# Kernel optimization log

Measured on AMD Instinct MI355X. Metric: run time of the kernel, lower is better.

## Reference

```python
import jax, jax.numpy as jnp
import numpy as np

EPS = 1e-05
H, N, F = 1024, 16, 4096  # hidden_dim, state_dim, ffn_dim


def layernorm(x, g, b):
    mu = jnp.mean(x, axis=-1, keepdims=True)
    var = jnp.mean(jnp.square(x - mu), axis=-1, keepdims=True)
    return (x - mu) * jax.lax.rsqrt(var + EPS) * g + b


def setup_inputs() -> dict:
    key = jax.random.key(0)
    ks = jax.random.split(key, 12)
    B, L = 2, 2048
    s = lambda fan_in: 1.0 / np.sqrt(fan_in)
    inp = {
        "x": jax.random.normal(ks[0], (B, L, H), jnp.float32),
        "ln1_g": jnp.ones((H,), jnp.float32),
        "ln1_b": jnp.zeros((H,), jnp.float32),
        "Wd": jax.random.uniform(ks[1], (H, H), jnp.float32, -s(H), s(H)),
        "bd": jnp.zeros((H,), jnp.float32),
        "Wbc": jax.random.uniform(ks[2], (2 * N, H), jnp.float32, -s(H), s(H)),
        "bbc": jnp.zeros((2 * N,), jnp.float32),
        "A_log": jnp.log(jnp.tile(jnp.arange(1, N + 1, dtype=jnp.float32), (H, 1))),
        "D": jnp.ones((H,), jnp.float32),
        "ln2_g": jnp.ones((H,), jnp.float32),
        "ln2_b": jnp.zeros((H,), jnp.float32),
        "W1": jax.random.uniform(ks[3], (F, H), jnp.float32, -s(H), s(H)),
        "b1": jnp.zeros((F,), jnp.float32),
        "W2": jax.random.uniform(ks[4], (H, F), jnp.float32, -s(F), s(F)),
        "b2": jnp.zeros((H,), jnp.float32),
    }
    return inp


def _selective_ssm(xn, delta, Bm, Cm, A, D):
    # xn: (B,L,H)  delta: (B,L,H)  Bm,Cm: (B,L,N)  A: (H,N)  D: (H,)
    Bsz = xn.shape[0]
    # time-major for scan
    xs = (jnp.moveaxis(delta, 1, 0), jnp.moveaxis(Bm, 1, 0),
          jnp.moveaxis(Cm, 1, 0), jnp.moveaxis(xn, 1, 0))

    def step(h, t):
        d_t, b_t, c_t, x_t = t  # (B,H), (B,N), (B,N), (B,H)
        dA = jnp.exp(d_t[:, :, None] * A)                      # (B,H,N)
        dBx = d_t[:, :, None] * b_t[:, None, :] * x_t[:, :, None]
        h = dA * h + dBx                                       # (B,H,N)
        y = jnp.einsum('bhn,bn->bh', h, c_t)                   # (B,H)
        return h, y

    h0 = jnp.zeros((Bsz, H, N), xn.dtype)
    _, ys = jax.lax.scan(step, h0, xs)
    y = jnp.moveaxis(ys, 0, 1)  # (B,L,H)
    return y + D * xn


def reference(x, ln1_g, ln1_b, Wd, bd, Wbc, bbc, A_log, D,
              ln2_g, ln2_b, W1, b1, W2, b2):
    # --- SSMLayer: pre-norm selective SSM + residual ---
    xn = layernorm(x, ln1_g, ln1_b)
    delta = jax.nn.softplus(xn @ Wd.T + bd)      # (B,L,H)
    bc = xn @ Wbc.T + bbc                        # (B,L,2N)
    Bm, Cm = bc[..., :N], bc[..., N:]
    A = -jnp.exp(A_log)                          # (H,N), negative real
    ssm_out = x + _selective_ssm(xn, delta, Bm, Cm, A, D)
    # --- MambaBlock: norm -> FFN -> residual with ssm_out ---
    normed = layernorm(ssm_out, ln2_g, ln2_b)
    hff = jax.nn.gelu(normed @ W1.T + b1, approximate=False)
    ffn_out = hff @ W2.T + b2
    return ffn_out + ssm_out
```

## Files before the change

### kernel.cpp

```cpp
#include <hip/hip_runtime.h>
#include <cstdint>
#include <cstddef>

typedef unsigned short USHORT;
typedef __bf16 bf16x8 __attribute__((ext_vector_type(8)));
typedef float f32x4 __attribute__((ext_vector_type(4)));

__device__ __forceinline__ float b2f(USHORT u) {
    union { unsigned int i; float f; } v; v.i = ((unsigned int)u) << 16; return v.f;
}
__device__ __forceinline__ USHORT f2bf(float f) {
    union { float f; unsigned int i; } v; v.f = f;
    unsigned int u = v.i;
    unsigned int r = (u + 0x7FFFu + ((u >> 16) & 1u)) >> 16;
    return (USHORT)r;
}
__device__ __forceinline__ float fexp2(float x) { return __builtin_amdgcn_exp2f(x); }

__device__ __forceinline__ void gload_lds16(const void* g, void* l) {
    __builtin_amdgcn_global_load_lds(
        (const __attribute__((address_space(1))) void*)(uintptr_t)g,
        (__attribute__((address_space(3))) void*)(uint32_t)(uintptr_t)l,
        16, 0, 0);
}

__global__ __launch_bounds__(256)
void f2b_kernel(const float* __restrict__ src, USHORT* __restrict__ dst, int n)
{
    int i = (blockIdx.x * 256 + threadIdx.x) * 4;
    if (i < n) {
        float4 v = *(const float4*)(src + i);
        ushort4 o;
        o.x = f2bf(v.x); o.y = f2bf(v.y); o.z = f2bf(v.z); o.w = f2bf(v.w);
        *(ushort4*)(dst + i) = o;
    }
}

__global__ __launch_bounds__(256)
void ln_kernel(const float* __restrict__ inp, const float* __restrict__ g,
               const float* __restrict__ bsh, USHORT* __restrict__ out)
{
    const int tid = threadIdx.x;
    const size_t row = blockIdx.x;
    float4 t = ((const float4*)inp)[row * 256 + tid];
    float v[4] = { t.x, t.y, t.z, t.w };
    float s = v[0] + v[1] + v[2] + v[3];
    float sq = v[0]*v[0] + v[1]*v[1] + v[2]*v[2] + v[3]*v[3];
    #pragma unroll
    for (int off = 32; off; off >>= 1) { s += __shfl_down(s, off); sq += __shfl_down(sq, off); }
    __shared__ float red[8];
    const int wv = tid >> 6;
    if ((tid & 63) == 0) { red[wv] = s; red[wv + 4] = sq; }
    __syncthreads();
    const float S  = red[0] + red[1] + red[2] + red[3];
    const float SQ = red[4] + red[5] + red[6] + red[7];
    const float mu = S * (1.0f / 1024.0f);
    const float var = SQ * (1.0f / 1024.0f) - mu * mu;
    const float rs = rsqrtf(var + 1e-5f);
    float4 gv = ((const float4*)g)[tid];
    float4 bv = ((const float4*)bsh)[tid];
    ushort4 o;
    o.x = f2bf((v[0] - mu) * rs * gv.x + bv.x);
    o.y = f2bf((v[1] - mu) * rs * gv.y + bv.y);
    o.z = f2bf((v[2] - mu) * rs * gv.z + bv.z);
    o.w = f2bf((v[3] - mu) * rs * gv.w + bv.w);
    ((ushort4*)out)[row * 256 + tid] = o;
}

template<int EPI>
__global__ __launch_bounds__(256)
void gemm_bt(const USHORT* __restrict__ A, const USHORT* __restrict__ B,
             const float* __restrict__ bias, void* __restrict__ outp,
             void* __restrict__ outp2, int M, int N, int K, int lda, int ldb)
{
    __shared__ __align__(16) unsigned char smem[32768];
    USHORT* As = (USHORT*)smem;
    USHORT* Bs = (USHORT*)(smem + 8192);
    const int tid = threadIdx.x;
    const int lane = tid & 63;
    const int w = tid >> 6;
    const int wr = w >> 1, wc = w & 1;

    const int nx = gridDim.x, ny = gridDim.y;
    const int pid = blockIdx.y * nx + blockIdx.x;
    const int npg = 8 * nx;
    const int gid = pid / npg;
    const int first = gid * 8;
    const int rem = ny - first;
    const int gsz = (rem < 8) ? rem : 8;
    const int py = first + (pid % npg) % gsz;
    const int px = (pid % npg) / gsz;
    const int tm = py * 128;
    const int tn = px * 128;

    f32x4 acc[4][4];
    #pragma unroll
    for (int i = 0; i < 4; i++)
        #pragma unroll
        for (int j = 0; j < 4; j++) acc[i][j] = (f32x4){0.f, 0.f, 0.f, 0.f};

    const int srow = tid >> 2;
    const int scol = (tid & 3) * 8;
    const USHORT* gA0 = A + (size_t)(tm + srow) * lda + scol;
    const USHORT* gA1 = A + (size_t)(tm + 64 + srow) * lda + scol;
    const USHORT* gB0 = B + (size_t)(tn + srow) * ldb + scol;
    const USHORT* gB1 = B + (size_t)(tn + 64 + srow) * ldb + scol;
    USHORT* lA0 = As + w * 512;
    USHORT* lA1 = As + 2048 + w * 512;
    USHORT* lB0 = Bs + w * 512;
    USHORT* lB1 = Bs + 2048 + w * 512;

    const int fr = lane & 15;
    const int fko = (lane >> 4) * 8;
    const int quad = lane >> 4;

    for (int k0 = 0; k0 < K; k0 += 64) {
        gload_lds16(gA0 + k0, lA0);
        gload_lds16(gA1 + k0, lA1);
        gload_lds16(gB0 + k0, lB0);
        gload_lds16(gB1 + k0, lB1);
        gload_lds16(gA0 + k0 + 32, lA0 + 8192);
        gload_lds16(gA1 + k0 + 32, lA1 + 8192);
        gload_lds16(gB0 + k0 + 32, lB0 + 8192);
        gload_lds16(gB1 + k0 + 32, lB1 + 8192);
        __syncthreads();
        #pragma unroll
        for (int h = 0; h < 2; h++) {
            const USHORT* Ah = As + h * 8192;
            const USHORT* Bh = Bs + h * 8192;
            bf16x8 af[4], bfr[4];
            #pragma unroll
            for (int i = 0; i < 4; i++) {
                af[i]  = *(const bf16x8*)(Ah + (wr * 64 + i * 16 + fr) * 32 + fko);
                bfr[i] = *(const bf16x8*)(Bh + (wc * 64 + i * 16 + fr) * 32 + fko);
            }
            #pragma unroll
            for (int i = 0; i < 4; i++)
                #pragma unroll
                for (int j = 0; j < 4; j++)
                    acc[i][j] = __builtin_amdgcn_mfma_f32_16x16x32_bf16(af[i], bfr[j], acc[i][j], 0, 0, 0);
        }
        __syncthreads();
    }

    float* eW = (float*)(smem + (size_t)w * 4352);
    const int rr = lane >> 5;
    const int cc = lane & 31;
    const int gcolb = tn + wc * 64;
    float2 bvv = *(const float2*)&bias[gcolb + cc * 2];

    #pragma unroll
    for (int i = 0; i < 4; i++) {
        #pragma unroll
        for (int j = 0; j < 4; j++)
            #pragma unroll
            for (int r = 0; r < 4; r++)
                eW[(quad * 4 + r) * 68 + j * 16 + fr] = acc[i][j][r];
        __syncthreads();
        const int grow0 = tm + wr * 64 + i * 16;
        #pragma unroll
        for (int rp = 0; rp < 8; rp++) {
            const int row = rp * 2 + rr;
            const float2 v = *(const float2*)&eW[row * 68 + cc * 2];
            const size_t gidx = (size_t)(grow0 + row) * N + gcolb + cc * 2;
            if constexpr (EPI == 2) {
                const float z0 = v.x + bvv.x, z1 = v.y + bvv.y;
                const float o0 = (z0 > 20.f) ? z0 : 0.69314718f * __log2f(1.f + fexp2(z0 * 1.44269504f));
                const float o1 = (z1 > 20.f) ? z1 : 0.69314718f * __log2f(1.f + fexp2(z1 * 1.44269504f));
                *(float2*)((float*)outp + gidx) = make_float2(o0, o1);
            }
        }
        __syncthreads();
    }
    (void)outp2; (void)M;
}

template<int EPI>
__global__ __launch_bounds__(512)
void gemm256(const USHORT* __restrict__ A, const USHORT* __restrict__ B,
             const float* __restrict__ bias, void* __restrict__ outp,
             void* __restrict__ outp2, int M, int N, int K, int lda, int ldb)
{
    __shared__ __align__(16) unsigned char smem[131072];
    const int tid = threadIdx.x;
    const int lane = tid & 63;
    const int w = tid >> 6;
    const int wr = w >> 2;
    const int wc = w & 3;

    const int gx = gridDim.x;
    const int pid = blockIdx.y * gx + blockIdx.x;
    const int nwg = gx * gridDim.y;
    const int cpx = nwg >> 3;
    const int s = (pid & 7) * cpx + (pid >> 3);
    const int px = s % gx;
    const int py = s / gx;
    const int tm = py * 256;
    const int tn = px * 256;

    USHORT* po = nullptr;
    if constexpr (EPI == 3) {
        const int z = blockIdx.z;
        A += (size_t)z * K;
        B += (size_t)z * K;
        po = ((z < 2) ? (USHORT*)outp : (USHORT*)outp2) + (size_t)(z & 1) * ((size_t)M * N);
    }

    const int sr = tid >> 2;
    const int su = (tid & 3) ^ ((tid >> 3) & 3);
    const USHORT* gA0 = A + (size_t)(tm + sr) * lda + su * 8;
    const USHORT* gA1 = A + (size_t)(tm + 128 + sr) * lda + su * 8;
    const USHORT* gB0 = B + (size_t)(tn + sr) * ldb + su * 8;
    const USHORT* gB1 = B + (size_t)(tn + 128 + sr) * ldb + su * 8;

    const int fr = lane & 15;
    const int quad = lane >> 4;
    const int uR = quad ^ ((fr >> 1) & 3);
    const int loff = fr * 32 + uR * 8;

    f32x4 acc[8][4];
    #pragma unroll
    for (int i = 0; i < 8; i++)
        #pragma unroll
        for (int j = 0; j < 4; j++) acc[i][j] = (f32x4){0.f, 0.f, 0.f, 0.f};

    const int NT = K >> 5;

    auto stage = [&](int t) {
        unsigned char* sb = smem + (size_t)(t & 3) * 32768;
        const size_t koff = (size_t)t * 32;
        gload_lds16(gA0 + koff, sb + w * 1024);
        gload_lds16(gA1 + koff, sb + 8192 + w * 1024);
        gload_lds16(gB0 + koff, sb + 16384 + w * 1024);
        gload_lds16(gB1 + koff, sb + 24576 + w * 1024);
    };

    stage(0);
    stage(1);

    for (int t = 0; t < NT; ++t) {
        if (t + 1 < NT) asm volatile("s_waitcnt vmcnt(4)" ::: "memory");
        else            asm volatile("s_waitcnt vmcnt(0)" ::: "memory");
        __builtin_amdgcn_s_barrier();
        if (t + 2 < NT) stage(t + 2);

        const USHORT* sA = (const USHORT*)(smem + (size_t)(t & 3) * 32768);
        const USHORT* sB = sA + 8192;
        bf16x8 a[4], b[4];
        #pragma unroll
        for (int j = 0; j < 4; j++)
            b[j] = *(const bf16x8*)(sB + (wc * 64 + j * 16) * 32 + loff);
        #pragma unroll
        for (int i = 0; i < 4; i++)
            a[i] = *(const bf16x8*)(sA + (wr * 128 + i * 16) * 32 + loff);
        __builtin_amdgcn_s_setprio(1);
        #pragma unroll
        for (int i = 0; i < 4; i++)
            #pragma unroll
            for (int j = 0; j < 4; j++)
                acc[i][j] = __builtin_amdgcn_mfma_f32_16x16x32_bf16(a[i], b[j], acc[i][j], 0, 0, 0);
        __builtin_amdgcn_s_setprio(0);
        #pragma unroll
        for (int i = 0; i < 4; i++)
            a[i] = *(const bf16x8*)(sA + (wr * 128 + 64 + i * 16) * 32 + loff);
        __builtin_amdgcn_s_setprio(1);
        #pragma unroll
        for (int i = 0; i < 4; i++)
            #pragma unroll
            for (int j = 0; j < 4; j++)
                acc[4 + i][j] = __builtin_amdgcn_mfma_f32_16x16x32_bf16(a[i], b[j], acc[4 + i][j], 0, 0, 0);
        __builtin_amdgcn_s_setprio(0);
    }

    float* eW = (float*)(smem + (size_t)w * 4352);
    const int erow = lane >> 2;
    const int ecq = lane & 3;
    const int gcolb = tn + wc * 64 + ecq * 16;
    float bb[16];
    if constexpr (EPI == 1) {
        #pragma unroll
        for (int q = 0; q < 4; q++) {
            float4 bv = *(const float4*)&bias[gcolb + q * 4];
            bb[q*4+0] = bv.x; bb[q*4+1] = bv.y; bb[q*4+2] = bv.z; bb[q*4+3] = bv.w;
        }
    }
    #pragma unroll
    for (int i = 0; i < 8; i++) {
        #pragma unroll
        for (int j = 0; j < 4; j++)
            #pragma unroll
            for (int r = 0; r < 4; r++)
                eW[(quad * 4 + r) * 68 + j * 16 + fr] = acc[i][j][r];
        float v[16];
        #pragma unroll
        for (int q = 0; q < 4; q++) {
            float4 t4 = *(const float4*)&eW[erow * 68 + ecq * 16 + q * 4];
            v[q*4+0] = t4.x; v[q*4+1] = t4.y; v[q*4+2] = t4.z; v[q*4+3] = t4.w;
        }
        const int grow = tm + wr * 128 + i * 16 + erow;
        uint32_t pk[8];
        if constexpr (EPI == 1) {
            #pragma unroll
            for (int q = 0; q < 8; q++) {
                const float z0 = v[2*q]   + bb[2*q];
                const float z1 = v[2*q+1] + bb[2*q+1];
                const float u0 = z0 * (0.7978845608f + 0.035677408f * z0 * z0);
                const float u1 = z1 * (0.7978845608f + 0.035677408f * z1 * z1);
                const float s0 = __builtin_amdgcn_rcpf(1.f + fexp2(2.885390082f * u0));
                const float s1 = __builtin_amdgcn_rcpf(1.f + fexp2(2.885390082f * u1));
                const float g0 = z0 * (1.f - s0), g1 = z1 * (1.f - s1);
                pk[q] = (uint32_t)f2bf(g0) | ((uint32_t)f2bf(g1) << 16);
            }
            USHORT* op = (USHORT*)outp + (size_t)grow * N + gcolb;
            *(uint4*)op = make_uint4(pk[0], pk[1], pk[2], pk[3]);
            *(uint4*)(op + 8) = make_uint4(pk[4], pk[5], pk[6], pk[7]);
        } else {
            #pragma unroll
            for (int q = 0; q < 8; q++)
                pk[q] = (uint32_t)f2bf(v[2*q]) | ((uint32_t)f2bf(v[2*q+1]) << 16);
            USHORT* op = po + (size_t)grow * N + gcolb;
            *(uint4*)op = make_uint4(pk[0], pk[1], pk[2], pk[3]);
            *(uint4*)(op + 8) = make_uint4(pk[4], pk[5], pk[6], pk[7]);
        }
    }
}

template<int EPI>
__global__ __launch_bounds__(512)
void gemm_tlp(const USHORT* __restrict__ A, const USHORT* __restrict__ B,
              const float* __restrict__ bias, void* __restrict__ outp,
              void* __restrict__ outp2, int M, int N, int K, int lda, int ldb)
{
    __shared__ __align__(16) unsigned char smem[73728];
    const int tid = threadIdx.x;
    const int lane = tid & 63;
    const int w = tid >> 6;
    const int wr = w >> 2;
    const int wc = w & 3;

    const int gx = gridDim.x;
    const int pid = blockIdx.y * gx + blockIdx.x;
    const int nwg = gx * gridDim.y;
    const int cpx = nwg >> 3;
    const int sw = (pid & 7) * cpx + (pid >> 3);
    const int tm = (sw % gx) * 128;
    const int tn = (sw / gx) * 256;

    USHORT* po = nullptr;
    if constexpr (EPI == 3) {
        const int z = blockIdx.z;
        A += (size_t)z * K;
        B += (size_t)z * K;
        po = ((z < 2) ? (USHORT*)outp : (USHORT*)outp2) + (size_t)(z & 1) * ((size_t)M * N);
    }

    const int srow = tid >> 2;
    const int su = (tid & 3) ^ ((tid >> 3) & 3);
    const USHORT* gA  = A + (size_t)(tm + srow) * lda + su * 8;
    const USHORT* gB0 = B + (size_t)(tn + srow) * ldb + su * 8;
    const USHORT* gB1 = B + (size_t)(tn + 128 + srow) * ldb + su * 8;

    const int fr = lane & 15;
    const int quad = lane >> 4;
    const int uR = quad ^ ((fr >> 1) & 3);
    const int loff = fr * 32 + uR * 8;

    f32x4 acc[4][4];
    #pragma unroll
    for (int i = 0; i < 4; i++)
        #pragma unroll
        for (int j = 0; j < 4; j++) acc[i][j] = (f32x4){0.f, 0.f, 0.f, 0.f};

    const int NT = K >> 5;

    auto stage = [&](int t) {
        unsigned char* sb = smem + (size_t)(t % 3) * 24576;
        const size_t ko = (size_t)t * 32;
        gload_lds16(gA  + ko, sb +         w * 1024);
        gload_lds16(gB0 + ko, sb +  8192 + w * 1024);
        gload_lds16(gB1 + ko, sb + 16384 + w * 1024);
    };

    stage(0);
    stage(1);

    for (int t = 0; t < NT; ++t) {
        if (t + 2 < NT) { stage(t + 2); asm volatile("s_waitcnt vmcnt(6)" ::: "memory"); }
        else if (t + 1 < NT) asm volatile("s_waitcnt vmcnt(3)" ::: "memory");
        else                 asm volatile("s_waitcnt vmcnt(0)" ::: "memory");
        __builtin_amdgcn_s_barrier();

        const USHORT* sA = (const USHORT*)(smem + (size_t)(t % 3) * 24576);
        const USHORT* sB = sA + 4096;
        bf16x8 a[4], b[4];
        #pragma unroll
        for (int j = 0; j < 4; j++)
            b[j] = *(const bf16x8*)(sB + (wc * 64 + j * 16) * 32 + loff);
        #pragma unroll
        for (int i = 0; i < 4; i++)
            a[i] = *(const bf16x8*)(sA + (wr * 64 + i * 16) * 32 + loff);
        __builtin_amdgcn_s_setprio(1);
        #pragma unroll
        for (int i = 0; i < 4; i++)
            #pragma unroll
            for (int j = 0; j < 4; j++)
                acc[i][j] = __builtin_amdgcn_mfma_f32_16x16x32_bf16(a[i], b[j], acc[i][j], 0, 0, 0);
        __builtin_amdgcn_s_setprio(0);
        __builtin_amdgcn_s_barrier();
    }

    __syncthreads();
    float* eW = (float*)(smem + (size_t)w * 4352);
    const int erow = lane >> 2;
    const int ecq = lane & 3;
    const int gcolb = tn + wc * 64 + ecq * 16;
    float bb[16];
    if constexpr (EPI == 1) {
        #pragma unroll
        for (int q = 0; q < 4; q++) {
            float4 bv = *(const float4*)&bias[gcolb + q * 4];
            bb[q*4+0] = bv.x; bb[q*4+1] = bv.y; bb[q*4+2] = bv.z; bb[q*4+3] = bv.w;
        }
    }
    #pragma unroll
    for (int i = 0; i < 4; i++) {
        #pragma unroll
        for (int j = 0; j < 4; j++)
            #pragma unroll
            for (int r = 0; r < 4; r++)
                eW[(quad * 4 + r) * 68 + j * 16 + fr] = acc[i][j][r];
        float v[16];
        #pragma unroll
        for (int q = 0; q < 4; q++) {
            float4 t4 = *(const float4*)&eW[erow * 68 + ecq * 16 + q * 4];
            v[q*4+0] = t4.x; v[q*4+1] = t4.y; v[q*4+2] = t4.z; v[q*4+3] = t4.w;
        }
        const int grow = tm + wr * 64 + i * 16 + erow;
        uint32_t pk[8];
        if constexpr (EPI == 1) {
            #pragma unroll
            for (int q = 0; q < 8; q++) {
                const float z0 = v[2*q]   + bb[2*q];
                const float z1 = v[2*q+1] + bb[2*q+1];
                const float u0 = z0 * (0.7978845608f + 0.035677408f * z0 * z0);
                const float u1 = z1 * (0.7978845608f + 0.035677408f * z1 * z1);
                const float s0 = __builtin_amdgcn_rcpf(1.f + fexp2(2.885390082f * u0));
                const float s1 = __builtin_amdgcn_rcpf(1.f + fexp2(2.885390082f * u1));
                const float g0 = z0 * (1.f - s0), g1 = z1 * (1.f - s1);
                pk[q] = (uint32_t)f2bf(g0) | ((uint32_t)f2bf(g1) << 16);
            }
            USHORT* op = (USHORT*)outp + (size_t)grow * N + gcolb;
            *(uint4*)op = make_uint4(pk[0], pk[1], pk[2], pk[3]);
            *(uint4*)(op + 8) = make_uint4(pk[4], pk[5], pk[6], pk[7]);
        } else {
            #pragma unroll
            for (int q = 0; q < 8; q++)
                pk[q] = (uint32_t)f2bf(v[2*q]) | ((uint32_t)f2bf(v[2*q+1]) << 16);
            USHORT* op = po + (size_t)grow * N + gcolb;
            *(uint4*)op = make_uint4(pk[0], pk[1], pk[2], pk[3]);
            *(uint4*)(op + 8) = make_uint4(pk[4], pk[5], pk[6], pk[7]);
        }
    }
    (void)bias;
}

__global__ __launch_bounds__(256)
void ffn2_reduce(const USHORT* __restrict__ p01, const USHORT* __restrict__ p23,
                 const float* __restrict__ bias, const float* __restrict__ extra,
                 float* __restrict__ out)
{
    const size_t PS = (size_t)4096 * 1024;
    const size_t i = ((size_t)blockIdx.x * 256 + threadIdx.x) * 4;
    ushort4 a = *(const ushort4*)(p01 + i);
    ushort4 b = *(const ushort4*)(p01 + PS + i);
    ushort4 c = *(const ushort4*)(p23 + i);
    ushort4 d = *(const ushort4*)(p23 + PS + i);
    float4 bv = *(const float4*)(bias + (i & 1023));
    float4 ev = *(const float4*)(extra + i);
    float4 o;
    o.x = b2f(a.x) + b2f(b.x) + b2f(c.x) + b2f(d.x) + bv.x + ev.x;
    o.y = b2f(a.y) + b2f(b.y) + b2f(c.y) + b2f(d.y) + bv.y + ev.y;
    o.z = b2f(a.z) + b2f(b.z) + b2f(c.z) + b2f(d.z) + bv.z + ev.z;
    o.w = b2f(a.w) + b2f(b.w) + b2f(c.w) + b2f(d.w) + bv.w + ev.w;
    *(float4*)(out + i) = o;
}

__global__ __launch_bounds__(256)
void bc_mfma(const USHORT* __restrict__ xn, const USHORT* __restrict__ WbcB,
             const float* __restrict__ bbc, float* __restrict__ bc)
{
    __shared__ __align__(16) USHORT As[64 * 32];
    __shared__ __align__(16) USHORT Bs[32 * 32];
    const int tid = threadIdx.x;
    const int lane = tid & 63;
    const int w = tid >> 6;
    const int tok0 = blockIdx.x * 64;

    const int srow = tid >> 2;
    const int scol = (tid & 3) * 8;
    const USHORT* gA = xn + (size_t)(tok0 + srow) * 1024 + scol;
    const USHORT* gB = WbcB + (size_t)srow * 1024 + scol;
    USHORT* lA = As + w * 512;
    USHORT* lB = Bs + w * 512;

    const int fr = lane & 15;
    const int fko = (lane >> 4) * 8;
    const int quad = lane >> 4;

    f32x4 acc[2];
    acc[0] = (f32x4){0.f, 0.f, 0.f, 0.f};
    acc[1] = (f32x4){0.f, 0.f, 0.f, 0.f};

    for (int k0 = 0; k0 < 1024; k0 += 32) {
        gload_lds16(gA + k0, lA);
        if (w < 2) gload_lds16(gB + k0, lB);
        __syncthreads();
        bf16x8 af = *(const bf16x8*)(As + (w * 16 + fr) * 32 + fko);
        bf16x8 b0 = *(const bf16x8*)(Bs + (fr) * 32 + fko);
        bf16x8 b1 = *(const bf16x8*)(Bs + (16 + fr) * 32 + fko);
        acc[0] = __builtin_amdgcn_mfma_f32_16x16x32_bf16(af, b0, acc[0], 0, 0, 0);
        acc[1] = __builtin_amdgcn_mfma_f32_16x16x32_bf16(af, b1, acc[1], 0, 0, 0);
        __syncthreads();
    }

    #pragma unroll
    for (int j = 0; j < 2; j++) {
        const int col = j * 16 + fr;
        const float bv = bbc[col];
        #pragma unroll
        for (int r = 0; r < 4; r++) {
            const int row = tok0 + w * 16 + quad * 4 + r;
            bc[(size_t)row * 32 + col] = acc[j][r] + bv;
        }
    }
}

#define SCAN_P 64
#define SCAN_T 32

__global__ __launch_bounds__(256)
void scan_pass1(const USHORT* __restrict__ xn, const float* __restrict__ delta,
                const float* __restrict__ bc, const float* __restrict__ Alog,
                float* __restrict__ sEnd, float* __restrict__ Ptot)
{
    const int tid = threadIdx.x;
    const int h = blockIdx.x * 256 + tid;
    const int b = blockIdx.y;
    const int p = blockIdx.z;
    const size_t tok0 = (size_t)b * 2048 + p * SCAN_T;

    __shared__ __align__(16) float sBC[SCAN_T][32];
    {
        int t = tid >> 3, q = (tid & 7) * 4;
        *(float4*)&sBC[t][q] = *(const float4*)(bc + (tok0 + t) * 32 + q);
    }

    float en[16], s[16], P[16];
    #pragma unroll
    for (int k = 0; k < 4; k++) {
        float4 a = *(const float4*)(Alog + h * 16 + k * 4);
        en[k*4+0] = -__expf(a.x) * 1.44269504f;
        en[k*4+1] = -__expf(a.y) * 1.44269504f;
        en[k*4+2] = -__expf(a.z) * 1.44269504f;
        en[k*4+3] = -__expf(a.w) * 1.44269504f;
    }
    #pragma unroll
    for (int n = 0; n < 16; n++) { s[n] = 0.f; P[n] = 1.f; }
    __syncthreads();

    const float* dp = delta + tok0 * 1024 + h;
    const USHORT* xp = xn + tok0 * 1024 + h;
    float d_c = dp[0];
    USHORT x_c = xp[0];
    for (int t = 0; t < SCAN_T; ++t) {
        const int tn = (t < SCAN_T - 1) ? t + 1 : t;
        float d_n = dp[(size_t)tn * 1024];
        USHORT x_n = xp[(size_t)tn * 1024];
        const float dx = d_c * b2f(x_c);
        #pragma unroll
        for (int k = 0; k < 4; k++) {
            float4 Bv = *(const float4*)&sBC[t][k*4];
            float bb[4] = { Bv.x, Bv.y, Bv.z, Bv.w };
            #pragma unroll
            for (int j = 0; j < 4; j++) {
                const int n = k*4 + j;
                const float dA = fexp2(d_c * en[n]);
                s[n] = fmaf(dA, s[n], dx * bb[j]);
                P[n] *= dA;
            }
        }
        d_c = d_n; x_c = x_n;
    }

    const size_t off = (size_t)p * 32768 + ((size_t)b * 1024 + h) * 16;
    #pragma unroll
    for (int k = 0; k < 4; k++) {
        *(float4*)(sEnd + off + k*4) = (float4){ s[k*4], s[k*4+1], s[k*4+2], s[k*4+3] };
        *(float4*)(Ptot + off + k*4) = (float4){ P[k*4], P[k*4+1], P[k*4+2], P[k*4+3] };
    }
}

__global__ __launch_bounds__(256)
void scan_mid(const float* __restrict__ sEnd, const float* __restrict__ Ptot,
              float* __restrict__ sIn)
{
    const int L = blockIdx.x * 256 + threadIdx.x;
    float s = 0.f;
    #pragma unroll 8
    for (int p = 0; p < SCAN_P; ++p) {
        const size_t off = (size_t)p * 32768 + L;
        sIn[off] = s;
        s = fmaf(Ptot[off], s, sEnd[off]);
    }
}

__global__ __launch_bounds__(256)
void scan_pass2(const float* __restrict__ x, const USHORT* __restrict__ xn,
                const float* __restrict__ delta, const float* __restrict__ bc,
                const float* __restrict__ Alog, const float* __restrict__ Dp,
                const float* __restrict__ sIn, float* __restrict__ ssm)
{
    const int tid = threadIdx.x;
    const int h = blockIdx.x * 256 + tid;
    const int b = blockIdx.y;
    const int p = blockIdx.z;
    const size_t tok0 = (size_t)b * 2048 + p * SCAN_T;

    __shared__ __align__(16) float sBC[SCAN_T][32];
    {
        int t = tid >> 3, q = (tid & 7) * 4;
        *(float4*)&sBC[t][q] = *(const float4*)(bc + (tok0 + t) * 32 + q);
    }

    float en[16], s[16];
    #pragma unroll
    for (int k = 0; k < 4; k++) {
        float4 a = *(const float4*)(Alog + h * 16 + k * 4);
        en[k*4+0] = -__expf(a.x) * 1.44269504f;
        en[k*4+1] = -__expf(a.y) * 1.44269504f;
        en[k*4+2] = -__expf(a.z) * 1.44269504f;
        en[k*4+3] = -__expf(a.w) * 1.44269504f;
    }
    const size_t off = (size_t)p * 32768 + ((size_t)b * 1024 + h) * 16;
    #pragma unroll
    for (int k = 0; k < 4; k++) {
        float4 v = *(const float4*)(sIn + off + k*4);
        s[k*4] = v.x; s[k*4+1] = v.y; s[k*4+2] = v.z; s[k*4+3] = v.w;
    }
    const float Dv = Dp[h];
    __syncthreads();

    const float* dp = delta + tok0 * 1024 + h;
    const USHORT* xp = xn + tok0 * 1024 + h;
    const float* xrp = x + tok0 * 1024 + h;
    float* op = ssm + tok0 * 1024 + h;

    float d_c = dp[0];
    USHORT x_c = xp[0];
    float xr_c = xrp[0];
    for (int t = 0; t < SCAN_T; ++t) {
        const int tn = (t < SCAN_T - 1) ? t + 1 : t;
        float d_n = dp[(size_t)tn * 1024];
        USHORT x_n = xp[(size_t)tn * 1024];
        float xr_n = xrp[(size_t)tn * 1024];
        const float xv = b2f(x_c);
        const float dx = d_c * xv;
        float y = 0.f;
        #pragma unroll
        for (int k = 0; k < 4; k++) {
            float4 Bv = *(const float4*)&sBC[t][k*4];
            float4 Cv = *(const float4*)&sBC[t][16 + k*4];
            float bb[4] = { Bv.x, Bv.y, Bv.z, Bv.w };
            float cc[4] = { Cv.x, Cv.y, Cv.z, Cv.w };
            #pragma unroll
            for (int j = 0; j < 4; j++) {
                const int n = k*4 + j;
                const float dA = fexp2(d_c * en[n]);
                s[n] = fmaf(dA, s[n], dx * bb[j]);
                y = fmaf(cc[j], s[n], y);
            }
        }
        op[(size_t)t * 1024] = xr_c + y + Dv * xv;
        d_c = d_n; x_c = x_n; xr_c = xr_n;
    }
}

extern "C" void kernel_launch(void* const* d_in, const int* in_sizes, int n_in,
                              void* d_out, int out_size, void* d_ws, size_t ws_size,
                              hipStream_t stream)
{
    const float* x    = (const float*)d_in[0];
    const float* ln1g = (const float*)d_in[1];
    const float* ln1b = (const float*)d_in[2];
    const float* Wd   = (const float*)d_in[3];
    const float* bd   = (const float*)d_in[4];
    const float* Wbc  = (const float*)d_in[5];
    const float* bbc  = (const float*)d_in[6];
    const float* Alog = (const float*)d_in[7];
    const float* Dp   = (const float*)d_in[8];
    const float* ln2g = (const float*)d_in[9];
    const float* ln2b = (const float*)d_in[10];
    const float* W1   = (const float*)d_in[11];
    const float* b1   = (const float*)d_in[12];
    const float* W2   = (const float*)d_in[13];
    const float* b2   = (const float*)d_in[14];
    float* out = (float*)d_out;

    char* ws = (char*)d_ws;
    const size_t MB = 1024 * 1024;
    float*  deltaW = (float*)(ws + 0);
    float*  ssmW   = (float*)(ws + 16 * MB);
    USHORT* xnW    = (USHORT*)(ws + 32 * MB);
    USHORT* nrmW   = (USHORT*)(ws + 40 * MB);
    USHORT* hffW   = (USHORT*)(ws + 48 * MB);
    float*  bcW    = (float*)(ws + 80 * MB);
    USHORT* WdB    = (USHORT*)(ws + 81 * MB);
    USHORT* W1B    = (USHORT*)(ws + 83 * MB);
    USHORT* W2B    = (USHORT*)(ws + 91 * MB);
    USHORT* WbcB   = (USHORT*)(ws + 99 * MB);
    float*  sEndW  = (float*)(ws + 48 * MB);
    float*  PtotW  = (float*)(ws + 56 * MB);
    float*  sInW   = (float*)(ws + 64 * MB);
    USHORT* ffn2p01 = (USHORT*)(ws + 0);
    USHORT* ffn2p23 = (USHORT*)(ws + 32 * MB);

    f2b_kernel<<<1024, 256, 0, stream>>>(Wd, WdB, 1024 * 1024);
    f2b_kernel<<<4096, 256, 0, stream>>>(W1, W1B, 4096 * 1024);
    f2b_kernel<<<4096, 256, 0, stream>>>(W2, W2B, 1024 * 4096);
    f2b_kernel<<<32, 256, 0, stream>>>(Wbc, WbcB, 32 * 1024);
    ln_kernel<<<4096, 256, 0, stream>>>(x, ln1g, ln1b, xnW);
    gemm_bt<2><<<dim3(8, 32), 256, 0, stream>>>(xnW, WdB, bd, deltaW, nullptr, 4096, 1024, 1024, 1024, 1024);
    bc_mfma<<<64, 256, 0, stream>>>(xnW, WbcB, bbc, bcW);
    scan_pass1<<<dim3(4, 2, SCAN_P), 256, 0, stream>>>(xnW, deltaW, bcW, Alog, sEndW, PtotW);
    scan_mid<<<128, 256, 0, stream>>>(sEndW, PtotW, sInW);
    scan_pass2<<<dim3(4, 2, SCAN_P), 256, 0, stream>>>(x, xnW, deltaW, bcW, Alog, Dp, sInW, ssmW);
    ln_kernel<<<4096, 256, 0, stream>>>(ssmW, ln2g, ln2b, nrmW);
    gemm256<1><<<dim3(16, 16), 512, 0, stream>>>(nrmW, W1B, b1, hffW, nullptr, 4096, 4096, 1024, 1024, 1024);
    gemm_tlp<3><<<dim3(32, 4, 4), 512, 0, stream>>>(hffW, W2B, nullptr, ffn2p01, ffn2p23, 4096, 1024, 1024, 4096, 4096);
    ffn2_reduce<<<4096, 256, 0, stream>>>(ffn2p01, ffn2p23, b2, ssmW, out);

    (void)in_sizes; (void)n_in; (void)out_size; (void)ws_size;
}
```

Measured before the change: 315.3 us.

## Merge weight casts, wave-per-row layernorm, halve FFN2 split-K, pipeline bc GEMM

Merges the four weight-to-bf16 conversion launches into one kernel. Layernorm now gives each wavefront its own row, which removes the shared-memory reduction and the block barrier. FFN2 split-K drops from four partials to two, so the reduce kernel reads half as many bf16 partial buffers, at the cost of fewer blocks and longer K loops in the GEMM. The small B/C projection moves to 16-token blocks with double-buffered async LDS loads, but only one wave issues MFMAs.

```diff
diff --git a/kernel.cpp b/kernel.cpp
--- a/kernel.cpp
+++ b/kernel.cpp
@@ -25,15 +25,22 @@
 }
 
 __global__ __launch_bounds__(256)
-void f2b_kernel(const float* __restrict__ src, USHORT* __restrict__ dst, int n)
-{
-    int i = (blockIdx.x * 256 + threadIdx.x) * 4;
-    if (i < n) {
-        float4 v = *(const float4*)(src + i);
-        ushort4 o;
-        o.x = f2bf(v.x); o.y = f2bf(v.y); o.z = f2bf(v.z); o.w = f2bf(v.w);
-        *(ushort4*)(dst + i) = o;
-    }
+void f2b_all(const float* __restrict__ Wd, const float* __restrict__ W1,
+             const float* __restrict__ W2, const float* __restrict__ Wbc,
+             USHORT* __restrict__ WdB, USHORT* __restrict__ W1B,
+             USHORT* __restrict__ W2B, USHORT* __restrict__ WbcB)
+{
+    const size_t u = (size_t)blockIdx.x * 256 + threadIdx.x;
+    const float* src; USHORT* dst; size_t base;
+    if (u < 262144)       { src = Wd;  dst = WdB;  base = 0; }
+    else if (u < 1310720) { src = W1;  dst = W1B;  base = 262144; }
+    else if (u < 2359296) { src = W2;  dst = W2B;  base = 1310720; }
+    else                  { src = Wbc; dst = WbcB; base = 2359296; }
+    const size_t i = (u - base) * 4;
+    float4 v = *(const float4*)(src + i);
+    ushort4 o;
+    o.x = f2bf(v.x); o.y = f2bf(v.y); o.z = f2bf(v.z); o.w = f2bf(v.w);
+    *(ushort4*)(dst + i) = o;
 }
 
 __global__ __launch_bounds__(256)
@@ -41,30 +48,34 @@
                const float* __restrict__ bsh, USHORT* __restrict__ out)
 {
     const int tid = threadIdx.x;
-    const size_t row = blockIdx.x;
-    float4 t = ((const float4*)inp)[row * 256 + tid];
-    float v[4] = { t.x, t.y, t.z, t.w };
-    float s = v[0] + v[1] + v[2] + v[3];
-    float sq = v[0]*v[0] + v[1]*v[1] + v[2]*v[2] + v[3]*v[3];
-    #pragma unroll
-    for (int off = 32; off; off >>= 1) { s += __shfl_down(s, off); sq += __shfl_down(sq, off); }
-    __shared__ float red[8];
-    const int wv = tid >> 6;
-    if ((tid & 63) == 0) { red[wv] = s; red[wv + 4] = sq; }
-    __syncthreads();
-    const float S  = red[0] + red[1] + red[2] + red[3];
-    const float SQ = red[4] + red[5] + red[6] + red[7];
-    const float mu = S * (1.0f / 1024.0f);
-    const float var = SQ * (1.0f / 1024.0f) - mu * mu;
+    const int lane = tid & 63;
+    const size_t row = (size_t)blockIdx.x * 4 + (tid >> 6);
+    const float4* ip = (const float4*)inp + row * 256;
+    float4 v[4];
+    float s = 0.f, sq = 0.f;
+    #pragma unroll
+    for (int q = 0; q < 4; q++) {
+        v[q] = ip[lane + 64 * q];
+        s  += v[q].x + v[q].y + v[q].z + v[q].w;
+        sq += v[q].x*v[q].x + v[q].y*v[q].y + v[q].z*v[q].z + v[q].w*v[q].w;
+    }
+    #pragma unroll
+    for (int off = 32; off; off >>= 1) { s += __shfl_xor(s, off); sq += __shfl_xor(sq, off); }
+    const float mu = s * (1.0f / 1024.0f);
+    const float var = sq * (1.0f / 1024.0f) - mu * mu;
     const float rs = rsqrtf(var + 1e-5f);
-    float4 gv = ((const float4*)g)[tid];
-    float4 bv = ((const float4*)bsh)[tid];
-    ushort4 o;
-    o.x = f2bf((v[0] - mu) * rs * gv.x + bv.x);
-    o.y = f2bf((v[1] - mu) * rs * gv.y + bv.y);
-    o.z = f2bf((v[2] - mu) * rs * gv.z + bv.z);
-    o.w = f2bf((v[3] - mu) * rs * gv.w + bv.w);
-    ((ushort4*)out)[row * 256 + tid] = o;
+    ushort4* op = (ushort4*)out + row * 256;
+    #pragma unroll
+    for (int q = 0; q < 4; q++) {
+        float4 gv = ((const float4*)g)[lane + 64 * q];
+        float4 bv = ((const float4*)bsh)[lane + 64 * q];
+        ushort4 o;
+        o.x = f2bf((v[q].x - mu) * rs * gv.x + bv.x);
+        o.y = f2bf((v[q].y - mu) * rs * gv.y + bv.y);
+        o.z = f2bf((v[q].z - mu) * rs * gv.z + bv.z);
+        o.w = f2bf((v[q].w - mu) * rs * gv.w + bv.w);
+        op[lane + 64 * q] = o;
+    }
 }
 
 template<int EPI>
@@ -465,23 +476,20 @@
 }
 
 __global__ __launch_bounds__(256)
-void ffn2_reduce(const USHORT* __restrict__ p01, const USHORT* __restrict__ p23,
-                 const float* __restrict__ bias, const float* __restrict__ extra,
-                 float* __restrict__ out)
+void ffn2_reduce(const USHORT* __restrict__ p, const float* __restrict__ bias,
+                 const float* __restrict__ extra, float* __restrict__ out)
 {
     const size_t PS = (size_t)4096 * 1024;
     const size_t i = ((size_t)blockIdx.x * 256 + threadIdx.x) * 4;
-    ushort4 a = *(const ushort4*)(p01 + i);
-    ushort4 b = *(const ushort4*)(p01 + PS + i);
-    ushort4 c = *(const ushort4*)(p23 + i);
-    ushort4 d = *(const ushort4*)(p23 + PS + i);
+    ushort4 a = *(const ushort4*)(p + i);
+    ushort4 b = *(const ushort4*)(p + PS + i);
     float4 bv = *(const float4*)(bias + (i & 1023));
     float4 ev = *(const float4*)(extra + i);
     float4 o;
-    o.x = b2f(a.x) + b2f(b.x) + b2f(c.x) + b2f(d.x) + bv.x + ev.x;
-    o.y = b2f(a.y) + b2f(b.y) + b2f(c.y) + b2f(d.y) + bv.y + ev.y;
-    o.z = b2f(a.z) + b2f(b.z) + b2f(c.z) + b2f(d.z) + bv.z + ev.z;
-    o.w = b2f(a.w) + b2f(b.w) + b2f(c.w) + b2f(d.w) + bv.w + ev.w;
+    o.x = b2f(a.x) + b2f(b.x) + bv.x + ev.x;
+    o.y = b2f(a.y) + b2f(b.y) + bv.y + ev.y;
+    o.z = b2f(a.z) + b2f(b.z) + bv.z + ev.z;
+    o.w = b2f(a.w) + b2f(b.w) + bv.w + ev.w;
     *(float4*)(out + i) = o;
 }
 
@@ -489,48 +497,57 @@
 void bc_mfma(const USHORT* __restrict__ xn, const USHORT* __restrict__ WbcB,
              const float* __restrict__ bbc, float* __restrict__ bc)
 {
-    __shared__ __align__(16) USHORT As[64 * 32];
-    __shared__ __align__(16) USHORT Bs[32 * 32];
+    __shared__ __align__(16) USHORT Bs[2][32 * 32];
+    __shared__ __align__(16) USHORT As[2][16 * 32];
     const int tid = threadIdx.x;
     const int lane = tid & 63;
     const int w = tid >> 6;
-    const int tok0 = blockIdx.x * 64;
-
-    const int srow = tid >> 2;
-    const int scol = (tid & 3) * 8;
-    const USHORT* gA = xn + (size_t)(tok0 + srow) * 1024 + scol;
-    const USHORT* gB = WbcB + (size_t)srow * 1024 + scol;
-    USHORT* lA = As + w * 512;
-    USHORT* lB = Bs + w * 512;
+    const int tok0 = blockIdx.x * 16;
 
     const int fr = lane & 15;
     const int fko = (lane >> 4) * 8;
     const int quad = lane >> 4;
 
+    const int srow = lane >> 2;
+    const int scol = (lane & 3) * 8;
+    const USHORT* gsrc = nullptr;
+    USHORT* ld0 = nullptr; USHORT* ld1 = nullptr;
+    if (w == 0)      { gsrc = WbcB + (size_t)srow * 1024 + scol;         ld0 = &Bs[0][0];   ld1 = &Bs[1][0]; }
+    else if (w == 1) { gsrc = WbcB + (size_t)(16 + srow) * 1024 + scol;  ld0 = &Bs[0][512]; ld1 = &Bs[1][512]; }
+    else if (w == 2) { gsrc = xn + (size_t)(tok0 + srow) * 1024 + scol;  ld0 = &As[0][0];   ld1 = &As[1][0]; }
+
     f32x4 acc[2];
     acc[0] = (f32x4){0.f, 0.f, 0.f, 0.f};
     acc[1] = (f32x4){0.f, 0.f, 0.f, 0.f};
 
-    for (int k0 = 0; k0 < 1024; k0 += 32) {
-        gload_lds16(gA + k0, lA);
-        if (w < 2) gload_lds16(gB + k0, lB);
+    if (w < 3) gload_lds16(gsrc, ld0);
+    for (int t = 0; t < 32; ++t) {
+        if (t + 1 < 32) {
+            if (w < 3) gload_lds16(gsrc + (t + 1) * 32, ((t + 1) & 1) ? ld1 : ld0);
+            asm volatile("s_waitcnt vmcnt(1)" ::: "memory");
+        } else {
+            asm volatile("s_waitcnt vmcnt(0)" ::: "memory");
+        }
         __syncthreads();
-        bf16x8 af = *(const bf16x8*)(As + (w * 16 + fr) * 32 + fko);
-        bf16x8 b0 = *(const bf16x8*)(Bs + (fr) * 32 + fko);
-        bf16x8 b1 = *(const bf16x8*)(Bs + (16 + fr) * 32 + fko);
-        acc[0] = __builtin_amdgcn_mfma_f32_16x16x32_bf16(af, b0, acc[0], 0, 0, 0);
-        acc[1] = __builtin_amdgcn_mfma_f32_16x16x32_bf16(af, b1, acc[1], 0, 0, 0);
-        __syncthreads();
-    }
-
-    #pragma unroll
-    for (int j = 0; j < 2; j++) {
-        const int col = j * 16 + fr;
-        const float bv = bbc[col];
-        #pragma unroll
-        for (int r = 0; r < 4; r++) {
-            const int row = tok0 + w * 16 + quad * 4 + r;
-            bc[(size_t)row * 32 + col] = acc[j][r] + bv;
+        if (w == 0) {
+            const USHORT* Ab = &As[t & 1][0];
+            const USHORT* Bb = &Bs[t & 1][0];
+            bf16x8 af = *(const bf16x8*)(Ab + fr * 32 + fko);
+            bf16x8 b0 = *(const bf16x8*)(Bb + fr * 32 + fko);
+            bf16x8 b1 = *(const bf16x8*)(Bb + (16 + fr) * 32 + fko);
+            acc[0] = __builtin_amdgcn_mfma_f32_16x16x32_bf16(af, b0, acc[0], 0, 0, 0);
+            acc[1] = __builtin_amdgcn_mfma_f32_16x16x32_bf16(af, b1, acc[1], 0, 0, 0);
+        }
+    }
+
+    if (w == 0) {
+        #pragma unroll
+        for (int j = 0; j < 2; j++) {
+            const int col = j * 16 + fr;
+            const float bv = bbc[col];
+            #pragma unroll
+            for (int r = 0; r < 4; r++)
+                bc[(size_t)(tok0 + quad * 4 + r) * 32 + col] = acc[j][r] + bv;
         }
     }
 }
@@ -721,23 +738,19 @@
     float*  sEndW  = (float*)(ws + 48 * MB);
     float*  PtotW  = (float*)(ws + 56 * MB);
     float*  sInW   = (float*)(ws + 64 * MB);
-    USHORT* ffn2p01 = (USHORT*)(ws + 0);
-    USHORT* ffn2p23 = (USHORT*)(ws + 32 * MB);
-
-    f2b_kernel<<<1024, 256, 0, stream>>>(Wd, WdB, 1024 * 1024);
-    f2b_kernel<<<4096, 256, 0, stream>>>(W1, W1B, 4096 * 1024);
-    f2b_kernel<<<4096, 256, 0, stream>>>(W2, W2B, 1024 * 4096);
-    f2b_kernel<<<32, 256, 0, stream>>>(Wbc, WbcB, 32 * 1024);
-    ln_kernel<<<4096, 256, 0, stream>>>(x, ln1g, ln1b, xnW);
+    USHORT* ffn2p  = (USHORT*)(ws + 0);
+
+    f2b_all<<<9248, 256, 0, stream>>>(Wd, W1, W2, Wbc, WdB, W1B, W2B, WbcB);
+    ln_kernel<<<1024, 256, 0, stream>>>(x, ln1g, ln1b, xnW);
     gemm_bt<2><<<dim3(8, 32), 256, 0, stream>>>(xnW, WdB, bd, deltaW, nullptr, 4096, 1024, 1024, 1024, 1024);
-    bc_mfma<<<64, 256, 0, stream>>>(xnW, WbcB, bbc, bcW);
+    bc_mfma<<<256, 256, 0, stream>>>(xnW, WbcB, bbc, bcW);
     scan_pass1<<<dim3(4, 2, SCAN_P), 256, 0, stream>>>(xnW, deltaW, bcW, Alog, sEndW, PtotW);
     scan_mid<<<128, 256, 0, stream>>>(sEndW, PtotW, sInW);
     scan_pass2<<<dim3(4, 2, SCAN_P), 256, 0, stream>>>(x, xnW, deltaW, bcW, Alog, Dp, sInW, ssmW);
-    ln_kernel<<<4096, 256, 0, stream>>>(ssmW, ln2g, ln2b, nrmW);
+    ln_kernel<<<1024, 256, 0, stream>>>(ssmW, ln2g, ln2b, nrmW);
     gemm256<1><<<dim3(16, 16), 512, 0, stream>>>(nrmW, W1B, b1, hffW, nullptr, 4096, 4096, 1024, 1024, 1024);
-    gemm_tlp<3><<<dim3(32, 4, 4), 512, 0, stream>>>(hffW, W2B, nullptr, ffn2p01, ffn2p23, 4096, 1024, 1024, 4096, 4096);
-    ffn2_reduce<<<4096, 256, 0, stream>>>(ffn2p01, ffn2p23, b2, ssmW, out);
+    gemm_tlp<3><<<dim3(32, 4, 2), 512, 0, stream>>>(hffW, W2B, nullptr, ffn2p, nullptr, 4096, 1024, 2048, 4096, 4096);
+    ffn2_reduce<<<4096, 256, 0, stream>>>(ffn2p, b2, ssmW, out);
 
     (void)in_sizes; (void)n_in; (void)out_size; (void)ws_size;
 }
```

Result: faster. 294.7 us, median of 2 (-6.5%).
